# Performance work log

Measured on AMD Instinct MI355X. Metric: run time of the kernel, lower is better.

The kernel has to match this reference:

```python
import jax, jax.numpy as jnp
import numpy as np

B, L, D, H = 2, 2048, 1024, 16
HD = D // H
EPS = 1e-6

def _rms(x, w):
    return x * jax.lax.rsqrt(jnp.mean(x * x, axis=-1, keepdims=True) + EPS) * w

def _lin(x, w, b=None):
    y = x @ w.T
    return y if b is None else y + b

def setup_inputs() -> dict:
    key = jax.random.key(0)
    ks = jax.random.split(key, 16)
    def w(i, shape, s=0.02):
        return jax.random.normal(ks[i], shape, dtype=jnp.float32) * s
    return dict(
        z=jax.random.normal(ks[0], (B, L, D), dtype=jnp.float32),
        connection=jax.random.normal(ks[1], (B, L, D), dtype=jnp.float32),
        w_z=jnp.ones(D, jnp.float32), w_c=jnp.ones(D, jnp.float32), w_mlp=jnp.ones(D, jnp.float32),
        f_w1=w(2, (2 * D, D)), f_b1=jnp.zeros(2 * D, jnp.float32),
        f_w2=w(3, (D, 2 * D)), f_b2=jnp.zeros(D, jnp.float32),
        g_w1=w(4, (D, 2 * D)), g_b1=jnp.zeros(D, jnp.float32),
        g_w2=w(5, (D, D)), g_b2=jnp.zeros(D, jnp.float32),
        dt=jnp.float32(0.1),
        q_w=w(6, (D, 2 * D)), k_w=w(7, (D, 2 * D)), v_w=w(8, (D, D)), o_w=w(9, (D, D)),
        temp=jnp.float32(1.0),
        cu_w1=w(10, (2 * D, 3 * D)), cu_b1=jnp.zeros(2 * D, jnp.float32),
        cu_w2=w(11, (D, 2 * D)), cu_b2=jnp.zeros(D, jnp.float32),
        m_w1=w(12, (4 * D, D)), m_b1=jnp.zeros(4 * D, jnp.float32),
        m_w2=w(13, (D, 4 * D)), m_b2=jnp.zeros(D, jnp.float32),
    )

def reference(z, connection, w_z, w_c, w_mlp,
              f_w1, f_b1, f_w2, f_b2, g_w1, g_b1, g_w2, g_b2, dt,
              q_w, k_w, v_w, o_w, temp,
              cu_w1, cu_b1, cu_w2, cu_b2,
              m_w1, m_b1, m_w2, m_b2):
    z_before = z
    zn = _rms(z, w_z)
    cn = _rms(connection, w_c)

    # covariant vector field: dz = dt * (F(zn) + gamma(cat(cn, F(zn))))
    dz_local = _lin(jax.nn.silu(_lin(zn, f_w1, f_b1)), f_w2, f_b2)
    corr = _lin(jnp.tanh(_lin(jnp.concatenate([cn, dz_local], -1), g_w1, g_b1)), g_w2, g_b2)
    dz = dt * (dz_local + corr)

    # covariant sigmoid attention
    zc = jnp.concatenate([zn, cn], -1)                       # [B,L,2D]
    Q = _lin(zc, q_w).reshape(B, L, H, HD).transpose(0, 2, 1, 3)  # bhld
    K = _lin(zc, k_w).reshape(B, L, H, HD).transpose(0, 2, 1, 3)
    V = _lin(zn, v_w).reshape(B, L, H, HD).transpose(0, 2, 1, 3)
    scores = jnp.einsum('bhld,bhmd->bhlm', Q, K) * (HD ** -0.5) * temp
    rel = jax.nn.sigmoid(scores)
    rel_sum = jnp.clip(jnp.sum(rel, -1, keepdims=True), 1.0, None)
    attn = jnp.einsum('bhlm,bhmd->bhld', rel, V) / rel_sum
    ctx = _lin(attn.transpose(0, 2, 1, 3).reshape(B, L, D), o_w)

    z1 = z + dz + ctx

    # connection update
    delta = _lin(jax.nn.silu(_lin(jnp.concatenate([connection, z1, dz], -1), cu_w1, cu_b1)), cu_w2, cu_b2)
    conn_new = connection + delta

    # MLP block
    z2 = z1 + _lin(jax.nn.silu(_lin(_rms(z1, w_mlp), m_w1, m_b1)), m_w2, m_b2)
    return (z2, conn_new, z_before)
```

## Files before the change

kernel.cpp:

```cpp
#include <hip/hip_runtime.h>


typedef unsigned short u16;
typedef __attribute__((ext_vector_type(8))) short short8;
typedef __attribute__((ext_vector_type(8))) unsigned short us8;
typedef __attribute__((ext_vector_type(4))) float f32x4;
typedef __attribute__((ext_vector_type(4))) unsigned short us4;

__device__ __forceinline__ float b2f(u16 u) {
    union { unsigned u; float f; } c; c.u = ((unsigned)u) << 16; return c.f;
}
__device__ __forceinline__ u16 f2b(float f) {
    union { float f; unsigned u; } c; c.f = f;
    unsigned x = c.u;
    unsigned r = (x + 0x7fffu + ((x >> 16) & 1u)) >> 16;
    return (u16)r;
}
__device__ __forceinline__ float fast_rcp(float x) {
    return __builtin_amdgcn_rcpf(x);
}

__device__ __forceinline__ void async_copy16(const u16* g, u16* l) {
    __builtin_amdgcn_global_load_lds(
        (const __attribute__((address_space(1))) unsigned int*)(g),
        (__attribute__((address_space(3))) unsigned int*)(l), 16, 0, 0);
}

__global__ __launch_bounds__(256) void cvt_k(const float* __restrict__ s,
                                             u16* __restrict__ d, int n) {
    int i = (blockIdx.x * 256 + threadIdx.x) * 4;
    if (i >= n) return;
    f32x4 v = *(const f32x4*)(s + i);
    us4 o;
#pragma unroll
    for (int k = 0; k < 4; k++) o[k] = f2b(v[k]);
    *(us4*)(d + i) = o;
}

__global__ __launch_bounds__(256) void rmsf_k(const float* __restrict__ x,
                                              const float* __restrict__ w,
                                              u16* __restrict__ y, int D) {
    int n = blockIdx.x;
    const float* xr = x + (size_t)n * D;
    int i0 = threadIdx.x << 2;
    f32x4 v = *(const f32x4*)(xr + i0);
    float s = v[0] * v[0] + v[1] * v[1] + v[2] * v[2] + v[3] * v[3];
#pragma unroll
    for (int m = 32; m >= 1; m >>= 1) s += __shfl_xor(s, m, 64);
    __shared__ float red[4];
    if ((threadIdx.x & 63) == 0) red[threadIdx.x >> 6] = s;
    __syncthreads();
    float tot = red[0] + red[1] + red[2] + red[3];
    float scale = rsqrtf(tot / (float)D + 1e-6f);
    f32x4 wv = *(const f32x4*)(w + i0);
    us4 o;
#pragma unroll
    for (int k = 0; k < 4; k++) o[k] = f2b(v[k] * scale * wv[k]);
    *(us4*)(y + (size_t)n * D + i0) = o;
}

__global__ __launch_bounds__(256) void rmsb_k(const u16* __restrict__ x,
                                              const float* __restrict__ w,
                                              u16* __restrict__ y, int D) {
    int n = blockIdx.x;
    const u16* xr = x + (size_t)n * D;
    int i0 = threadIdx.x << 2;
    us4 xv = *(const us4*)(xr + i0);
    float v[4]; float s = 0.f;
#pragma unroll
    for (int k = 0; k < 4; k++) { v[k] = b2f(xv[k]); s += v[k] * v[k]; }
#pragma unroll
    for (int m = 32; m >= 1; m >>= 1) s += __shfl_xor(s, m, 64);
    __shared__ float red[4];
    if ((threadIdx.x & 63) == 0) red[threadIdx.x >> 6] = s;
    __syncthreads();
    float tot = red[0] + red[1] + red[2] + red[3];
    float scale = rsqrtf(tot / (float)D + 1e-6f);
    f32x4 wv = *(const f32x4*)(w + i0);
    us4 o;
#pragma unroll
    for (int k = 0; k < 4; k++) o[k] = f2b(v[k] * scale * wv[k]);
    *(us4*)(y + (size_t)n * D + i0) = o;
}

template <int BN>
__global__ __launch_bounds__(256) void gemm_t(const u16* __restrict__ A,
                                              const u16* __restrict__ W,
                                              const float* __restrict__ bias,
                                              u16* __restrict__ C,
                                              int K, int O, int act, int mode) {
    constexpr int NJ = BN / 32;
    constexpr int WN = BN / 2;
    __shared__ u16 Asm[2][128 * 32];
    __shared__ u16 Bsm[2][BN * 32];

    const int tid = threadIdx.x;
    const int wid = tid >> 6, lane = tid & 63;
    const int l15 = lane & 15, quad = lane >> 4;
    const int row0 = blockIdx.y * 128, col0 = blockIdx.x * BN;
    const int wm = (wid >> 1) << 6, wn = (wid & 1) * WN;

    const int sr = tid >> 2;
    const int sc = tid & 3;
    const int ga = sc ^ ((sr ^ (sr >> 2)) & 3);
    const u16* aS0 = A + (size_t)(row0 + sr) * K + ga * 8;
    const u16* aS1 = A + (size_t)(row0 + 64 + sr) * K + ga * 8;
    const u16* bS0 = W + (size_t)(col0 + sr) * K + ga * 8;
    const u16* bS1 = W + (size_t)(col0 + 64 + sr) * K + ga * 8;

    const int qa = quad ^ ((l15 ^ (l15 >> 2)) & 3);

    f32x4 acc[4][NJ];
#pragma unroll
    for (int i = 0; i < 4; i++)
#pragma unroll
        for (int j = 0; j < NJ; j++) acc[i][j] = (f32x4){0.f, 0.f, 0.f, 0.f};

    const int wbs = wid << 9;
    auto stage = [&](int buf, int kof) {
        async_copy16(aS0 + kof, &Asm[buf][wbs]);
        async_copy16(aS1 + kof, &Asm[buf][2048 + wbs]);
        async_copy16(bS0 + kof, &Bsm[buf][wbs]);
        if constexpr (BN == 128) async_copy16(bS1 + kof, &Bsm[buf][2048 + wbs]);
    };

    const int nk = K >> 5;
    stage(0, 0);
    __syncthreads();
    for (int kk = 0; kk < nk; kk++) {
        int cur = kk & 1;
        if (kk + 1 < nk) stage(1 - cur, (kk + 1) << 5);
        const u16* Ab = Asm[cur];
        const u16* Bb = Bsm[cur];
        short8 af[4], bf[NJ];
#pragma unroll
        for (int i = 0; i < 4; i++)
            af[i] = *(const short8*)&Ab[(wm + i * 16 + l15) * 32 + qa * 8];
#pragma unroll
        for (int j = 0; j < NJ; j++)
            bf[j] = *(const short8*)&Bb[(wn + j * 16 + l15) * 32 + qa * 8];
#pragma unroll
        for (int i = 0; i < 4; i++)
#pragma unroll
            for (int j = 0; j < NJ; j++)
                acc[i][j] = __builtin_amdgcn_mfma_f32_16x16x32_bf16(af[i], bf[j], acc[i][j], 0, 0, 0);
        __syncthreads();
    }

    if (mode == 0) {
#pragma unroll
        for (int j = 0; j < NJ; j++) {
            int col = col0 + wn + j * 16 + l15;
            float bb = bias ? bias[col] : 0.f;
#pragma unroll
            for (int i = 0; i < 4; i++) {
                int rowb = row0 + wm + i * 16 + (quad << 2);
#pragma unroll
                for (int g = 0; g < 4; g++) {
                    float v = acc[i][j][g] + bb;
                    if (act == 1) {
                        v = v * fast_rcp(1.f + __expf(-v));
                    } else if (act == 2) {
                        float t = __expf(v * 2.f);
                        v = 1.f - 2.f * fast_rcp(1.f + t);
                    }
                    C[(size_t)(rowb + g) * O + col] = f2b(v);
                }
            }
        }
    } else {
#pragma unroll
        for (int j = 0; j < NJ; j++) {
            int col = col0 + wn + j * 16 + l15;
            int h = col >> 6, d = col & 63;
#pragma unroll
            for (int i = 0; i < 4; i++) {
                int rowb = row0 + wm + i * 16 + (quad << 2);
                int bb_ = rowb >> 11;
                int tok = rowb & 2047;
                us4 pk;
#pragma unroll
                for (int g = 0; g < 4; g++) pk[g] = f2b(acc[i][j][g]);
                *(us4*)&C[(size_t)(((bb_ << 4) + h) * 64 + d) * 2048 + tok] = pk;
            }
        }
    }
}

__global__ __launch_bounds__(256) void attn_k(const u16* __restrict__ Q,
                                              const u16* __restrict__ Kb,
                                              const u16* __restrict__ VT,
                                              const float* __restrict__ temp_p,
                                              u16* __restrict__ Oa) {
    const int L = 2048, H = 16, D = 1024;
    __shared__ u16 Ks[2][64 * 64];
    __shared__ u16 Vs[2][64 * 64];
    __shared__ u16 plds[4][16 * 72];

    const int tid = threadIdx.x;
    const int w = tid >> 6, lane = tid & 63;
    const int l15 = lane & 15, quad = lane >> 4;
    const int bh = blockIdx.x >> 4;
    const int qb0 = (blockIdx.x & 15) << 7;
    const int b = bh >> 4, h = bh & 15;
    const float nscale = -0.125f * temp_p[0];

    short8 aq[2][2];
#pragma unroll
    for (int qt = 0; qt < 2; qt++) {
        size_t row = (size_t)(b * L + qb0 + w * 32 + qt * 16 + l15) * D + h * 64;
#pragma unroll
        for (int hf = 0; hf < 2; hf++)
            aq[qt][hf] = *(const short8*)(Q + row + hf * 32 + quad * 8);
    }

    const u16* Kbase = Kb + (size_t)(b * L) * D + h * 64;
    const u16* VTb   = VT + (size_t)bh * 64 * L;

    const int i0 = tid, i1 = tid + 256;
    const int r0 = i0 >> 3, g0 = (i0 & 7) ^ (r0 & 7);
    const int r1 = i1 >> 3, g1 = (i1 & 7) ^ (r1 & 7);
    const u16* kS0 = Kbase + (size_t)r0 * D + g0 * 8;
    const u16* kS1 = Kbase + (size_t)r1 * D + g1 * 8;
    const u16* vS0 = VTb + (size_t)r0 * L + g0 * 8;
    const u16* vS1 = VTb + (size_t)r1 * L + g1 * 8;

    auto stage = [&](int buf, int mc) {
        async_copy16(kS0 + (size_t)mc * D, &Ks[buf][w << 9]);
        async_copy16(kS1 + (size_t)mc * D, &Ks[buf][2048 + (w << 9)]);
        async_copy16(vS0 + mc, &Vs[buf][w << 9]);
        async_copy16(vS1 + mc, &Vs[buf][2048 + (w << 9)]);
    };

    f32x4 acc[2][4];
#pragma unroll
    for (int i = 0; i < 2; i++)
#pragma unroll
        for (int j = 0; j < 4; j++) acc[i][j] = (f32x4){0.f, 0.f, 0.f, 0.f};
    float rs[2][4] = {{0.f,0.f,0.f,0.f},{0.f,0.f,0.f,0.f}};
    u16* P = plds[w];
    const int lsw = l15 & 7;

    stage(0, 0);
    __syncthreads();
    for (int it = 0; it < 32; it++) {
        int cur = it & 1;
        if (it < 31) stage(1 - cur, (it + 1) << 6);
        const u16* Kt = Ks[cur];
        const u16* Vt = Vs[cur];
#pragma unroll
        for (int qt = 0; qt < 2; qt++) {
#pragma unroll
            for (int ks = 0; ks < 4; ks++) {
                f32x4 s = (f32x4){0.f, 0.f, 0.f, 0.f};
#pragma unroll
                for (int hf = 0; hf < 2; hf++) {
                    int slot = ((ks * 16 + l15) * 8 + ((hf * 4 + quad) ^ lsw)) * 8;
                    short8 bk = *(const short8*)&Kt[slot];
                    s = __builtin_amdgcn_mfma_f32_16x16x32_bf16(aq[qt][hf], bk, s, 0, 0, 0);
                }
#pragma unroll
                for (int g = 0; g < 4; g++) {
                    float e = __expf(s[g] * nscale);
                    float p = fast_rcp(1.f + e);
                    rs[qt][g] += p;
                    P[(quad * 4 + g) * 72 + ks * 16 + l15] = f2b(p);
                }
            }
#pragma unroll
            for (int kh = 0; kh < 2; kh++) {
                short8 ap = *(const short8*)&P[l15 * 72 + kh * 32 + quad * 8];
#pragma unroll
                for (int dt = 0; dt < 4; dt++) {
                    int slot = ((dt * 16 + l15) * 8 + ((kh * 4 + quad) ^ lsw)) * 8;
                    short8 bv = *(const short8*)&Vt[slot];
                    acc[qt][dt] = __builtin_amdgcn_mfma_f32_16x16x32_bf16(ap, bv, acc[qt][dt], 0, 0, 0);
                }
            }
        }
        __syncthreads();
    }

#pragma unroll
    for (int qt = 0; qt < 2; qt++)
#pragma unroll
        for (int g = 0; g < 4; g++) {
#pragma unroll
            for (int m = 1; m < 16; m <<= 1) rs[qt][g] += __shfl_xor(rs[qt][g], m, 64);
        }

#pragma unroll
    for (int qt = 0; qt < 2; qt++) {
        u16* orow = Oa + (size_t)(b * L + qb0 + w * 32 + qt * 16) * D + h * 64;
#pragma unroll
        for (int g = 0; g < 4; g++) {
            float rd = fast_rcp(fmaxf(rs[qt][g], 1.0f));
            int row = quad * 4 + g;
#pragma unroll
            for (int dt = 0; dt < 4; dt++)
                orow[(size_t)row * D + dt * 16 + l15] = f2b(acc[qt][dt][g] * rd);
        }
    }
}

__global__ void concat2_k(u16* __restrict__ dst, const u16* __restrict__ s0,
                          const u16* __restrict__ s1, int total) {
    int i = (blockIdx.x * 256 + threadIdx.x) * 8;
    if (i >= total) return;
    int j = i & 1023;
    int t = i >> 10;
    int seg = t & 1;
    int n = t >> 1;
    const u16* s = seg ? s1 : s0;
    *(us8*)(dst + i) = *(const us8*)&s[(size_t)n * 1024 + j];
}

__global__ void cucat_k(u16* __restrict__ dst, const float* __restrict__ conn,
                        const u16* __restrict__ z1, const u16* __restrict__ dz,
                        int total) {
    int i = (blockIdx.x * 256 + threadIdx.x) * 8;
    if (i >= total) return;
    int j = i & 1023;
    int t = i >> 10;
    int seg = t % 3;
    int n = t / 3;
    size_t src = (size_t)n * 1024 + j;
    if (seg == 0) {
        f32x4 a = *(const f32x4*)(conn + src);
        f32x4 b = *(const f32x4*)(conn + src + 4);
        us8 o;
#pragma unroll
        for (int k = 0; k < 4; k++) { o[k] = f2b(a[k]); o[k + 4] = f2b(b[k]); }
        *(us8*)(dst + i) = o;
    } else {
        const u16* s = (seg == 1) ? z1 : dz;
        *(us8*)(dst + i) = *(const us8*)&s[src];
    }
}

__global__ void dz_k(u16* __restrict__ d, const u16* __restrict__ a,
                     const u16* __restrict__ b, const float* __restrict__ dtp, int n) {
    int i = (blockIdx.x * 256 + threadIdx.x) * 8;
    if (i >= n) return;
    float dt = dtp[0];
    us8 va = *(const us8*)(a + i), vb = *(const us8*)(b + i);
    us8 o;
#pragma unroll
    for (int k = 0; k < 8; k++) o[k] = f2b(dt * (b2f(va[k]) + b2f(vb[k])));
    *(us8*)(d + i) = o;
}

__global__ void z1_k(u16* __restrict__ d, const float* __restrict__ z,
                     const u16* __restrict__ dz, const u16* __restrict__ ctx, int n) {
    int i = (blockIdx.x * 256 + threadIdx.x) * 8;
    if (i >= n) return;
    f32x4 z0 = *(const f32x4*)(z + i), z4 = *(const f32x4*)(z + i + 4);
    us8 vd = *(const us8*)(dz + i), vc = *(const us8*)(ctx + i);
    us8 o;
#pragma unroll
    for (int k = 0; k < 4; k++) {
        o[k]     = f2b(z0[k] + b2f(vd[k])     + b2f(vc[k]));
        o[k + 4] = f2b(z4[k] + b2f(vd[k + 4]) + b2f(vc[k + 4]));
    }
    *(us8*)(d + i) = o;
}

__global__ void connew_k(float* __restrict__ d, const float* __restrict__ conn,
                         const u16* __restrict__ delta, int n) {
    int i = (blockIdx.x * 256 + threadIdx.x) * 8;
    if (i >= n) return;
    f32x4 c0 = *(const f32x4*)(conn + i), c4 = *(const f32x4*)(conn + i + 4);
    us8 vd = *(const us8*)(delta + i);
    f32x4 o0, o4;
#pragma unroll
    for (int k = 0; k < 4; k++) {
        o0[k] = c0[k] + b2f(vd[k]);
        o4[k] = c4[k] + b2f(vd[k + 4]);
    }
    *(f32x4*)(d + i) = o0;
    *(f32x4*)(d + i + 4) = o4;
}

__global__ void z2_k(float* __restrict__ d, const u16* __restrict__ z1,
                     const u16* __restrict__ mf, int n) {
    int i = (blockIdx.x * 256 + threadIdx.x) * 8;
    if (i >= n) return;
    us8 va = *(const us8*)(z1 + i), vb = *(const us8*)(mf + i);
    f32x4 o0, o4;
#pragma unroll
    for (int k = 0; k < 4; k++) {
        o0[k] = b2f(va[k]) + b2f(vb[k]);
        o4[k] = b2f(va[k + 4]) + b2f(vb[k + 4]);
    }
    *(f32x4*)(d + i) = o0;
    *(f32x4*)(d + i + 4) = o4;
}

__global__ void copyf_k(float* __restrict__ d, const float* __restrict__ s, int n) {
    int i = (blockIdx.x * 256 + threadIdx.x) * 4;
    if (i >= n) return;
    *(f32x4*)(d + i) = *(const f32x4*)(s + i);
}

extern "C" void kernel_launch(void* const* d_in, const int* in_sizes, int n_in,
                              void* d_out, int out_size, void* d_ws, size_t ws_size,
                              hipStream_t stream) {
    const int B = 2, L = 2048, D = 1024, H = 16, N = B * L;
    const float* z      = (const float*)d_in[0];
    const float* conn   = (const float*)d_in[1];
    const float* w_z    = (const float*)d_in[2];
    const float* w_c    = (const float*)d_in[3];
    const float* w_mlp  = (const float*)d_in[4];
    const float* f_w1   = (const float*)d_in[5];
    const float* f_b1   = (const float*)d_in[6];
    const float* f_w2   = (const float*)d_in[7];
    const float* f_b2   = (const float*)d_in[8];
    const float* g_w1   = (const float*)d_in[9];
    const float* g_b1   = (const float*)d_in[10];
    const float* g_w2   = (const float*)d_in[11];
    const float* g_b2   = (const float*)d_in[12];
    const float* dt_p   = (const float*)d_in[13];
    const float* q_w    = (const float*)d_in[14];
    const float* k_w    = (const float*)d_in[15];
    const float* v_w    = (const float*)d_in[16];
    const float* o_w    = (const float*)d_in[17];
    const float* temp_p = (const float*)d_in[18];
    const float* cu_w1  = (const float*)d_in[19];
    const float* cu_b1  = (const float*)d_in[20];
    const float* cu_w2  = (const float*)d_in[21];
    const float* cu_b2  = (const float*)d_in[22];
    const float* m_w1   = (const float*)d_in[23];
    const float* m_b1   = (const float*)d_in[24];
    const float* m_w2   = (const float*)d_in[25];
    const float* m_b2   = (const float*)d_in[26];

    float* out = (float*)d_out;
    u16* ws  = (u16*)d_ws;
    const size_t U = (size_t)N * D;

    u16* zn    = ws + 0 * U;
    u16* cn    = ws + 1 * U;
    u16* h1    = ws + 2 * U;
    u16* dzl   = ws + 4 * U;
    u16* gcat  = ws + 5 * U;
    u16* gh    = ws + 7 * U;
    u16* corr  = ws + 5 * U;
    u16* dz    = ws + 6 * U;
    u16* zc    = ws + 2 * U;
    u16* Qb    = ws + 4 * U;
    u16* Kbuf  = ws + 5 * U;
    u16* VT    = ws + 7 * U;
    u16* attn  = ws + 8 * U;
    u16* ctx   = ws + 4 * U;
    u16* z1    = ws + 5 * U;
    u16* cu_in = ws + 0 * U;
    u16* cu_h  = ws + 3 * U;
    u16* delta = ws + 7 * U;
    u16* z1n   = ws + 0 * U;
    u16* mh    = ws + 1 * U;
    u16* mf    = ws + 0 * U;

    u16* wb = ws + 9 * U;
    u16* bf_w1  = wb + 0;
    u16* bf_w2  = wb + 2 * 1024 * 1024;
    u16* bg_w1  = wb + 4 * 1024 * 1024;
    u16* bg_w2  = wb + 6 * 1024 * 1024;
    u16* bq_w   = wb + 7 * 1024 * 1024;
    u16* bk_w   = wb + 9 * 1024 * 1024;
    u16* bv_w   = wb + 11 * 1024 * 1024;
    u16* bo_w   = wb + 12 * 1024 * 1024;
    u16* bcu_w1 = wb + 13 * 1024 * 1024;
    u16* bcu_w2 = wb + 19 * 1024 * 1024;
    u16* bm_w1  = wb + 21 * 1024 * 1024;
    u16* bm_w2  = wb + 25 * 1024 * 1024;

    auto cvt = [&](const float* s, u16* d, int n) {
        cvt_k<<<n / 1024, 256, 0, stream>>>(s, d, n);
    };
    cvt(f_w1, bf_w1, 2 * D * D);   cvt(f_w2, bf_w2, 2 * D * D);
    cvt(g_w1, bg_w1, 2 * D * D);   cvt(g_w2, bg_w2, D * D);
    cvt(q_w, bq_w, 2 * D * D);     cvt(k_w, bk_w, 2 * D * D);
    cvt(v_w, bv_w, D * D);         cvt(o_w, bo_w, D * D);
    cvt(cu_w1, bcu_w1, 6 * D * D); cvt(cu_w2, bcu_w2, 2 * D * D);
    cvt(m_w1, bm_w1, 4 * D * D);   cvt(m_w2, bm_w2, 4 * D * D);

    const int EW8 = (N * D / 8 + 255) / 256;
    auto gemm = [&](const u16* A, const u16* W, const float* bias, u16* C,
                    int K, int O, int act, int mode = 0) {
        if (O == 1024) {
            dim3 grid(O / 64, N / 128);
            gemm_t<64><<<grid, 256, 0, stream>>>(A, W, bias, C, K, O, act, mode);
        } else {
            dim3 grid(O / 128, N / 128);
            gemm_t<128><<<grid, 256, 0, stream>>>(A, W, bias, C, K, O, act, mode);
        }
    };

    rmsf_k<<<N, 256, 0, stream>>>(z, w_z, zn, D);
    rmsf_k<<<N, 256, 0, stream>>>(conn, w_c, cn, D);

    gemm(zn, bf_w1, f_b1, h1, D, 2 * D, 1);
    gemm(h1, bf_w2, f_b2, dzl, 2 * D, D, 0);
    concat2_k<<<(N * 2 * D / 8 + 255) / 256, 256, 0, stream>>>(gcat, cn, dzl, N * 2 * D);
    gemm(gcat, bg_w1, g_b1, gh, 2 * D, D, 2);
    gemm(gh, bg_w2, g_b2, corr, D, D, 0);
    dz_k<<<EW8, 256, 0, stream>>>(dz, dzl, corr, dt_p, N * D);

    concat2_k<<<(N * 2 * D / 8 + 255) / 256, 256, 0, stream>>>(zc, zn, cn, N * 2 * D);
    gemm(zc, bq_w, nullptr, Qb, 2 * D, D, 0);
    gemm(zc, bk_w, nullptr, Kbuf, 2 * D, D, 0);
    gemm(zn, bv_w, nullptr, VT, D, D, 0, 1);
    attn_k<<<B * H * L / 128, 256, 0, stream>>>(Qb, Kbuf, VT, temp_p, attn);
    gemm(attn, bo_w, nullptr, ctx, D, D, 0);

    z1_k<<<EW8, 256, 0, stream>>>(z1, z, dz, ctx, N * D);

    cucat_k<<<(N * 3 * D / 8 + 255) / 256, 256, 0, stream>>>(cu_in, conn, z1, dz, N * 3 * D);
    gemm(cu_in, bcu_w1, cu_b1, cu_h, 3 * D, 2 * D, 1);
    gemm(cu_h, bcu_w2, cu_b2, delta, 2 * D, D, 0);
    connew_k<<<EW8, 256, 0, stream>>>(out + U, conn, delta, N * D);
    copyf_k<<<(N * D + 1023) / 1024, 256, 0, stream>>>(out + 2 * U, z, N * D);

    rmsb_k<<<N, 256, 0, stream>>>(z1, w_mlp, z1n, D);
    gemm(z1n, bm_w1, m_b1, mh, D, 4 * D, 1);
    gemm(mh, bm_w2, m_b2, mf, 4 * D, D, 0);
    z2_k<<<EW8, 256, 0, stream>>>(out, z1, mf, N * D);
}
```

Measured before the change: 880.3 us.

## Fuse concats into multi-segment GEMM loads, merge Q/K GEMM, widen K tile

The GEMM kernel now takes up to three A-operand segments, so the concatenation kernels for the gamma, Q/K and connection-update inputs are removed and each GEMM reads directly from the separate sources. Q and K projections are merged into one GEMM with concatenated weights, and the attention kernel reads both from the shared buffer. The GEMM K-tile grows from 32 to 64 with a new XOR swizzle, which halves the loop iterations and barriers but doubles LDS use. Attention switches to exp2 with packed bf16 conversion and a transposed MFMA so each lane keeps one row sum, and the z copy is folded into the RMS-norm kernel. Risks include the larger LDS footprint lowering occupancy and the hard-coded grid sizes depending on N.

Result: faster. 749.9 us (-14.8%).

```diff
diff --git a/kernel.cpp b/kernel.cpp
--- a/kernel.cpp
+++ b/kernel.cpp
@@ -6,6 +6,7 @@
 typedef __attribute__((ext_vector_type(8))) unsigned short us8;
 typedef __attribute__((ext_vector_type(4))) float f32x4;
 typedef __attribute__((ext_vector_type(4))) unsigned short us4;
+typedef __attribute__((ext_vector_type(2))) unsigned int u32x2;
 
 __device__ __forceinline__ float b2f(u16 u) {
     union { unsigned u; float f; } c; c.u = ((unsigned)u) << 16; return c.f;
@@ -18,6 +19,11 @@
 }
 __device__ __forceinline__ float fast_rcp(float x) {
     return __builtin_amdgcn_rcpf(x);
+}
+__device__ __forceinline__ unsigned cvt_pk_bf16(float a, float b) {
+    unsigned r;
+    asm("v_cvt_pk_bf16_f32 %0, %1, %2" : "=v"(r) : "v"(a), "v"(b));
+    return r;
 }
 
 __device__ __forceinline__ void async_copy16(const u16* g, u16* l) {
@@ -39,11 +45,13 @@
 
 __global__ __launch_bounds__(256) void rmsf_k(const float* __restrict__ x,
                                               const float* __restrict__ w,
-                                              u16* __restrict__ y, int D) {
+                                              u16* __restrict__ y,
+                                              float* __restrict__ cp, int D) {
     int n = blockIdx.x;
     const float* xr = x + (size_t)n * D;
     int i0 = threadIdx.x << 2;
     f32x4 v = *(const f32x4*)(xr + i0);
+    if (cp) *(f32x4*)(cp + (size_t)n * D + i0) = v;
     float s = v[0] * v[0] + v[1] * v[1] + v[2] * v[2] + v[3] * v[3];
 #pragma unroll
     for (int m = 32; m >= 1; m >>= 1) s += __shfl_xor(s, m, 64);
@@ -83,32 +91,32 @@
     *(us4*)(y + (size_t)n * D + i0) = o;
 }
 
-template <int BN>
-__global__ __launch_bounds__(256) void gemm_t(const u16* __restrict__ A,
+template <int BN, int NSEG>
+__global__ __launch_bounds__(256) void gemm_t(const u16* __restrict__ A0,
+                                              const u16* __restrict__ A1,
+                                              const u16* __restrict__ A2,
                                               const u16* __restrict__ W,
                                               const float* __restrict__ bias,
                                               u16* __restrict__ C,
                                               int K, int O, int act, int mode) {
     constexpr int NJ = BN / 32;
     constexpr int WN = BN / 2;
-    __shared__ u16 Asm[2][128 * 32];
-    __shared__ u16 Bsm[2][BN * 32];
+    __shared__ u16 Asm[2][128 * 64];
+    __shared__ u16 Bsm[2][BN * 64];
 
     const int tid = threadIdx.x;
     const int wid = tid >> 6, lane = tid & 63;
     const int l15 = lane & 15, quad = lane >> 4;
+    const int lsw = l15 & 7;
     const int row0 = blockIdx.y * 128, col0 = blockIdx.x * BN;
     const int wm = (wid >> 1) << 6, wn = (wid & 1) * WN;
 
-    const int sr = tid >> 2;
-    const int sc = tid & 3;
-    const int ga = sc ^ ((sr ^ (sr >> 2)) & 3);
-    const u16* aS0 = A + (size_t)(row0 + sr) * K + ga * 8;
-    const u16* aS1 = A + (size_t)(row0 + 64 + sr) * K + ga * 8;
-    const u16* bS0 = W + (size_t)(col0 + sr) * K + ga * 8;
-    const u16* bS1 = W + (size_t)(col0 + 64 + sr) * K + ga * 8;
-
-    const int qa = quad ^ ((l15 ^ (l15 >> 2)) & 3);
+    const int rb = tid >> 3;
+    const int gg = ((tid & 7) ^ (rb & 7)) << 3;
+    const int sA = (NSEG == 1) ? K : 1024;
+    const size_t aoff = (size_t)(row0 + rb) * sA + gg;
+    const size_t boff = (size_t)(col0 + rb) * K + gg;
+    const int ldsb = wid << 9;
 
     f32x4 acc[4][NJ];
 #pragma unroll
@@ -116,34 +124,48 @@
 #pragma unroll
         for (int j = 0; j < NJ; j++) acc[i][j] = (f32x4){0.f, 0.f, 0.f, 0.f};
 
-    const int wbs = wid << 9;
     auto stage = [&](int buf, int kof) {
-        async_copy16(aS0 + kof, &Asm[buf][wbs]);
-        async_copy16(aS1 + kof, &Asm[buf][2048 + wbs]);
-        async_copy16(bS0 + kof, &Bsm[buf][wbs]);
-        if constexpr (BN == 128) async_copy16(bS1 + kof, &Bsm[buf][2048 + wbs]);
+        const u16* Ab; int kcol;
+        if constexpr (NSEG == 1) { Ab = A0; kcol = kof; }
+        else {
+            int seg = kof >> 10;
+            Ab = (seg == 0) ? A0 : ((NSEG == 3 && seg == 2) ? A2 : A1);
+            kcol = kof & 1023;
+        }
+        const u16* as = Ab + aoff + kcol;
+        const u16* bs = W + boff + kof;
+#pragma unroll
+        for (int i = 0; i < 4; i++)
+            async_copy16(as + (size_t)(32 * i) * sA, &Asm[buf][(i << 11) + ldsb]);
+#pragma unroll
+        for (int i = 0; i < BN / 32; i++)
+            async_copy16(bs + (size_t)(32 * i) * K, &Bsm[buf][(i << 11) + ldsb]);
     };
 
-    const int nk = K >> 5;
+    const int nk = K >> 6;
     stage(0, 0);
     __syncthreads();
     for (int kk = 0; kk < nk; kk++) {
         int cur = kk & 1;
-        if (kk + 1 < nk) stage(1 - cur, (kk + 1) << 5);
+        if (kk + 1 < nk) stage(1 - cur, (kk + 1) << 6);
         const u16* Ab = Asm[cur];
         const u16* Bb = Bsm[cur];
-        short8 af[4], bf[NJ];
-#pragma unroll
-        for (int i = 0; i < 4; i++)
-            af[i] = *(const short8*)&Ab[(wm + i * 16 + l15) * 32 + qa * 8];
-#pragma unroll
-        for (int j = 0; j < NJ; j++)
-            bf[j] = *(const short8*)&Bb[(wn + j * 16 + l15) * 32 + qa * 8];
-#pragma unroll
-        for (int i = 0; i < 4; i++)
+#pragma unroll
+        for (int h = 0; h < 2; h++) {
+            const int gq = (((h << 2) + quad) ^ lsw) << 3;
+            short8 af[4], bf[NJ];
+#pragma unroll
+            for (int i = 0; i < 4; i++)
+                af[i] = *(const short8*)&Ab[(wm + i * 16 + l15) * 64 + gq];
 #pragma unroll
             for (int j = 0; j < NJ; j++)
-                acc[i][j] = __builtin_amdgcn_mfma_f32_16x16x32_bf16(af[i], bf[j], acc[i][j], 0, 0, 0);
+                bf[j] = *(const short8*)&Bb[(wn + j * 16 + l15) * 64 + gq];
+#pragma unroll
+            for (int i = 0; i < 4; i++)
+#pragma unroll
+                for (int j = 0; j < NJ; j++)
+                    acc[i][j] = __builtin_amdgcn_mfma_f32_16x16x32_bf16(af[i], bf[j], acc[i][j], 0, 0, 0);
+        }
         __syncthreads();
     }
 
@@ -187,12 +209,11 @@
     }
 }
 
-__global__ __launch_bounds__(256) void attn_k(const u16* __restrict__ Q,
-                                              const u16* __restrict__ Kb,
+__global__ __launch_bounds__(256) void attn_k(const u16* __restrict__ QK,
                                               const u16* __restrict__ VT,
                                               const float* __restrict__ temp_p,
                                               u16* __restrict__ Oa) {
-    const int L = 2048, H = 16, D = 1024;
+    const int L = 2048, D = 1024, SQ = 2048;
     __shared__ u16 Ks[2][64 * 64];
     __shared__ u16 Vs[2][64 * 64];
     __shared__ u16 plds[4][16 * 72];
@@ -203,31 +224,31 @@
     const int bh = blockIdx.x >> 4;
     const int qb0 = (blockIdx.x & 15) << 7;
     const int b = bh >> 4, h = bh & 15;
-    const float nscale = -0.125f * temp_p[0];
+    const float nsc2 = -0.125f * temp_p[0] * 1.44269504f;
 
     short8 aq[2][2];
 #pragma unroll
     for (int qt = 0; qt < 2; qt++) {
-        size_t row = (size_t)(b * L + qb0 + w * 32 + qt * 16 + l15) * D + h * 64;
+        size_t row = (size_t)(b * L + qb0 + w * 32 + qt * 16 + l15) * SQ + h * 64;
 #pragma unroll
         for (int hf = 0; hf < 2; hf++)
-            aq[qt][hf] = *(const short8*)(Q + row + hf * 32 + quad * 8);
-    }
-
-    const u16* Kbase = Kb + (size_t)(b * L) * D + h * 64;
+            aq[qt][hf] = *(const short8*)(QK + row + hf * 32 + quad * 8);
+    }
+
+    const u16* Kbase = QK + 1024 + (size_t)(b * L) * SQ + h * 64;
     const u16* VTb   = VT + (size_t)bh * 64 * L;
 
     const int i0 = tid, i1 = tid + 256;
     const int r0 = i0 >> 3, g0 = (i0 & 7) ^ (r0 & 7);
     const int r1 = i1 >> 3, g1 = (i1 & 7) ^ (r1 & 7);
-    const u16* kS0 = Kbase + (size_t)r0 * D + g0 * 8;
-    const u16* kS1 = Kbase + (size_t)r1 * D + g1 * 8;
+    const u16* kS0 = Kbase + (size_t)r0 * SQ + g0 * 8;
+    const u16* kS1 = Kbase + (size_t)r1 * SQ + g1 * 8;
     const u16* vS0 = VTb + (size_t)r0 * L + g0 * 8;
     const u16* vS1 = VTb + (size_t)r1 * L + g1 * 8;
 
     auto stage = [&](int buf, int mc) {
-        async_copy16(kS0 + (size_t)mc * D, &Ks[buf][w << 9]);
-        async_copy16(kS1 + (size_t)mc * D, &Ks[buf][2048 + (w << 9)]);
+        async_copy16(kS0 + (size_t)mc * SQ, &Ks[buf][w << 9]);
+        async_copy16(kS1 + (size_t)mc * SQ, &Ks[buf][2048 + (w << 9)]);
         async_copy16(vS0 + mc, &Vs[buf][w << 9]);
         async_copy16(vS1 + mc, &Vs[buf][2048 + (w << 9)]);
     };
@@ -237,7 +258,7 @@
     for (int i = 0; i < 2; i++)
 #pragma unroll
         for (int j = 0; j < 4; j++) acc[i][j] = (f32x4){0.f, 0.f, 0.f, 0.f};
-    float rs[2][4] = {{0.f,0.f,0.f,0.f},{0.f,0.f,0.f,0.f}};
+    float rs[2] = {0.f, 0.f};
     u16* P = plds[w];
     const int lsw = l15 & 7;
 
@@ -257,15 +278,17 @@
                 for (int hf = 0; hf < 2; hf++) {
                     int slot = ((ks * 16 + l15) * 8 + ((hf * 4 + quad) ^ lsw)) * 8;
                     short8 bk = *(const short8*)&Kt[slot];
-                    s = __builtin_amdgcn_mfma_f32_16x16x32_bf16(aq[qt][hf], bk, s, 0, 0, 0);
+                    s = __builtin_amdgcn_mfma_f32_16x16x32_bf16(bk, aq[qt][hf], s, 0, 0, 0);
                 }
-#pragma unroll
-                for (int g = 0; g < 4; g++) {
-                    float e = __expf(s[g] * nscale);
-                    float p = fast_rcp(1.f + e);
-                    rs[qt][g] += p;
-                    P[(quad * 4 + g) * 72 + ks * 16 + l15] = f2b(p);
-                }
+                float p0 = fast_rcp(1.f + __builtin_amdgcn_exp2f(s[0] * nsc2));
+                float p1 = fast_rcp(1.f + __builtin_amdgcn_exp2f(s[1] * nsc2));
+                float p2 = fast_rcp(1.f + __builtin_amdgcn_exp2f(s[2] * nsc2));
+                float p3 = fast_rcp(1.f + __builtin_amdgcn_exp2f(s[3] * nsc2));
+                rs[qt] += (p0 + p1) + (p2 + p3);
+                u32x2 pk2;
+                pk2[0] = cvt_pk_bf16(p0, p1);
+                pk2[1] = cvt_pk_bf16(p2, p3);
+                *(u32x2*)&P[l15 * 72 + ks * 16 + (quad << 2)] = pk2;
             }
 #pragma unroll
             for (int kh = 0; kh < 2; kh++) {
@@ -282,59 +305,23 @@
     }
 
 #pragma unroll
-    for (int qt = 0; qt < 2; qt++)
-#pragma unroll
-        for (int g = 0; g < 4; g++) {
-#pragma unroll
-            for (int m = 1; m < 16; m <<= 1) rs[qt][g] += __shfl_xor(rs[qt][g], m, 64);
-        }
+    for (int qt = 0; qt < 2; qt++) {
+        rs[qt] += __shfl_xor(rs[qt], 16, 64);
+        rs[qt] += __shfl_xor(rs[qt], 32, 64);
+    }
 
 #pragma unroll
     for (int qt = 0; qt < 2; qt++) {
         u16* orow = Oa + (size_t)(b * L + qb0 + w * 32 + qt * 16) * D + h * 64;
 #pragma unroll
         for (int g = 0; g < 4; g++) {
-            float rd = fast_rcp(fmaxf(rs[qt][g], 1.0f));
             int row = quad * 4 + g;
+            float denom = __shfl(rs[qt], row, 64);
+            float rd = fast_rcp(fmaxf(denom, 1.0f));
 #pragma unroll
             for (int dt = 0; dt < 4; dt++)
                 orow[(size_t)row * D + dt * 16 + l15] = f2b(acc[qt][dt][g] * rd);
         }
-    }
-}
-
-__global__ void concat2_k(u16* __restrict__ dst, const u16* __restrict__ s0,
-                          const u16* __restrict__ s1, int total) {
-    int i = (blockIdx.x * 256 + threadIdx.x) * 8;
-    if (i >= total) return;
-    int j = i & 1023;
-    int t = i >> 10;
-    int seg = t & 1;
-    int n = t >> 1;
-    const u16* s = seg ? s1 : s0;
-    *(us8*)(dst + i) = *(const us8*)&s[(size_t)n * 1024 + j];
-}
-
-__global__ void cucat_k(u16* __restrict__ dst, const float* __restrict__ conn,
-                        const u16* __restrict__ z1, const u16* __restrict__ dz,
-                        int total) {
-    int i = (blockIdx.x * 256 + threadIdx.x) * 8;
-    if (i >= total) return;
-    int j = i & 1023;
-    int t = i >> 10;
-    int seg = t % 3;
-    int n = t / 3;
-    size_t src = (size_t)n * 1024 + j;
-    if (seg == 0) {
-        f32x4 a = *(const f32x4*)(conn + src);
-        f32x4 b = *(const f32x4*)(conn + src + 4);
-        us8 o;
-#pragma unroll
-        for (int k = 0; k < 4; k++) { o[k] = f2b(a[k]); o[k + 4] = f2b(b[k]); }
-        *(us8*)(dst + i) = o;
-    } else {
-        const u16* s = (seg == 1) ? z1 : dz;
-        *(us8*)(dst + i) = *(const us8*)&s[src];
     }
 }
 
@@ -394,12 +381,6 @@
     }
     *(f32x4*)(d + i) = o0;
     *(f32x4*)(d + i + 4) = o4;
-}
-
-__global__ void copyf_k(float* __restrict__ d, const float* __restrict__ s, int n) {
-    int i = (blockIdx.x * 256 + threadIdx.x) * 4;
-    if (i >= n) return;
-    *(f32x4*)(d + i) = *(const f32x4*)(s + i);
 }
 
 extern "C" void kernel_launch(void* const* d_in, const int* in_sizes, int n_in,
@@ -442,31 +423,27 @@
     u16* cn    = ws + 1 * U;
     u16* h1    = ws + 2 * U;
     u16* dzl   = ws + 4 * U;
-    u16* gcat  = ws + 5 * U;
-    u16* gh    = ws + 7 * U;
-    u16* corr  = ws + 5 * U;
-    u16* dz    = ws + 6 * U;
-    u16* zc    = ws + 2 * U;
-    u16* Qb    = ws + 4 * U;
-    u16* Kbuf  = ws + 5 * U;
-    u16* VT    = ws + 7 * U;
-    u16* attn  = ws + 8 * U;
+    u16* gh    = ws + 5 * U;
+    u16* corr  = ws + 6 * U;
+    u16* dz    = ws + 7 * U;
+    u16* connb = ws + 8 * U;
+    u16* QK    = ws + 2 * U;
+    u16* VT    = ws + 4 * U;
+    u16* attnb = ws + 1 * U;
     u16* ctx   = ws + 4 * U;
     u16* z1    = ws + 5 * U;
-    u16* cu_in = ws + 0 * U;
-    u16* cu_h  = ws + 3 * U;
-    u16* delta = ws + 7 * U;
+    u16* cu_h  = ws + 2 * U;
+    u16* delta = ws + 1 * U;
     u16* z1n   = ws + 0 * U;
     u16* mh    = ws + 1 * U;
-    u16* mf    = ws + 0 * U;
+    u16* mf    = ws + 6 * U;
 
     u16* wb = ws + 9 * U;
     u16* bf_w1  = wb + 0;
     u16* bf_w2  = wb + 2 * 1024 * 1024;
     u16* bg_w1  = wb + 4 * 1024 * 1024;
     u16* bg_w2  = wb + 6 * 1024 * 1024;
-    u16* bq_w   = wb + 7 * 1024 * 1024;
-    u16* bk_w   = wb + 9 * 1024 * 1024;
+    u16* bqk_w  = wb + 7 * 1024 * 1024;
     u16* bv_w   = wb + 11 * 1024 * 1024;
     u16* bo_w   = wb + 12 * 1024 * 1024;
     u16* bcu_w1 = wb + 13 * 1024 * 1024;
@@ -479,47 +456,46 @@
     };
     cvt(f_w1, bf_w1, 2 * D * D);   cvt(f_w2, bf_w2, 2 * D * D);
     cvt(g_w1, bg_w1, 2 * D * D);   cvt(g_w2, bg_w2, D * D);
-    cvt(q_w, bq_w, 2 * D * D);     cvt(k_w, bk_w, 2 * D * D);
+    cvt(q_w, bqk_w, 2 * D * D);    cvt(k_w, bqk_w + 2 * D * D, 2 * D * D);
     cvt(v_w, bv_w, D * D);         cvt(o_w, bo_w, D * D);
     cvt(cu_w1, bcu_w1, 6 * D * D); cvt(cu_w2, bcu_w2, 2 * D * D);
     cvt(m_w1, bm_w1, 4 * D * D);   cvt(m_w2, bm_w2, 4 * D * D);
+    cvt(conn, connb, N * D);
 
     const int EW8 = (N * D / 8 + 255) / 256;
     auto gemm = [&](const u16* A, const u16* W, const float* bias, u16* C,
                     int K, int O, int act, int mode = 0) {
         if (O == 1024) {
-            dim3 grid(O / 64, N / 128);
-            gemm_t<64><<<grid, 256, 0, stream>>>(A, W, bias, C, K, O, act, mode);
+            dim3 grid(16, 32);
+            gemm_t<64, 1><<<grid, 256, 0, stream>>>(A, nullptr, nullptr, W, bias, C, K, O, act, mode);
         } else {
-            dim3 grid(O / 128, N / 128);
-            gemm_t<128><<<grid, 256, 0, stream>>>(A, W, bias, C, K, O, act, mode);
+            dim3 grid(O / 128, 32);
+            gemm_t<128, 1><<<grid, 256, 0, stream>>>(A, nullptr, nullptr, W, bias, C, K, O, act, mode);
         }
     };
 
-    rmsf_k<<<N, 256, 0, stream>>>(z, w_z, zn, D);
-    rmsf_k<<<N, 256, 0, stream>>>(conn, w_c, cn, D);
+    rmsf_k<<<N, 256, 0, stream>>>(z, w_z, zn, out + 2 * U, D);
+    rmsf_k<<<N, 256, 0, stream>>>(conn, w_c, cn, nullptr, D);
 
     gemm(zn, bf_w1, f_b1, h1, D, 2 * D, 1);
     gemm(h1, bf_w2, f_b2, dzl, 2 * D, D, 0);
-    concat2_k<<<(N * 2 * D / 8 + 255) / 256, 256, 0, stream>>>(gcat, cn, dzl, N * 2 * D);
-    gemm(gcat, bg_w1, g_b1, gh, 2 * D, D, 2);
+    gemm_t<64, 2><<<dim3(16, 32), 256, 0, stream>>>(
+        cn, dzl, nullptr, bg_w1, g_b1, gh, 2 * D, D, 2, 0);
     gemm(gh, bg_w2, g_b2, corr, D, D, 0);
     dz_k<<<EW8, 256, 0, stream>>>(dz, dzl, corr, dt_p, N * D);
 
-    concat2_k<<<(N * 2 * D / 8 + 255) / 256, 256, 0, stream>>>(zc, zn, cn, N * 2 * D);
-    gemm(zc, bq_w, nullptr, Qb, 2 * D, D, 0);
-    gemm(zc, bk_w, nullptr, Kbuf, 2 * D, D, 0);
+    gemm_t<128, 2><<<dim3(16, 32), 256, 0, stream>>>(
+        zn, cn, nullptr, bqk_w, nullptr, QK, 2 * D, 2 * D, 0, 0);
     gemm(zn, bv_w, nullptr, VT, D, D, 0, 1);
-    attn_k<<<B * H * L / 128, 256, 0, stream>>>(Qb, Kbuf, VT, temp_p, attn);
-    gemm(attn, bo_w, nullptr, ctx, D, D, 0);
+    attn_k<<<B * H * L / 128, 256, 0, stream>>>(QK, VT, temp_p, attnb);
+    gemm(attnb, bo_w, nullptr, ctx, D, D, 0);
 
     z1_k<<<EW8, 256, 0, stream>>>(z1, z, dz, ctx, N * D);
 
-    cucat_k<<<(N * 3 * D / 8 + 255) / 256, 256, 0, stream>>>(cu_in, conn, z1, dz, N * 3 * D);
-    gemm(cu_in, bcu_w1, cu_b1, cu_h, 3 * D, 2 * D, 1);
+    gemm_t<128, 3><<<dim3(16, 32), 256, 0, stream>>>(
+        connb, z1, dz, bcu_w1, cu_b1, cu_h, 3 * D, 2 * D, 1, 0);
     gemm(cu_h, bcu_w2, cu_b2, delta, 2 * D, D, 0);
     connew_k<<<EW8, 256, 0, stream>>>(out + U, conn, delta, N * D);
-    copyf_k<<<(N * D + 1023) / 1024, 256, 0, stream>>>(out + 2 * U, z, N * D);
 
     rmsb_k<<<N, 256, 0, stream>>>(z1, w_mlp, z1n, D);
     gemm(z1n, bm_w1, m_b1, mh, D, 4 * D, 1);
```
